# Performance work log

Hardware: AMD Instinct MI355X
Metric: run time of the kernel (lower is better)

Reference implementation:

```python
import jax, jax.numpy as jnp
import numpy as np

H = 512  # hidden size

def _lstm_layer(xseq, W_ih, W_hh, b_ih, b_hh):
    """xseq: [S,B,D]. Returns (h_seq [S,B,H], c_final [B,H]). PyTorch gate order i,f,g,o."""
    S, B, _ = xseq.shape
    # precompute input contribution for all timesteps: [S,B,4H]
    gx = jnp.einsum('sbd,gd->sbg', xseq, W_ih) + b_ih + b_hh
    h0 = jnp.zeros((B, H), xseq.dtype)
    c0 = jnp.zeros((B, H), xseq.dtype)

    def step(carry, gx_t):
        h, c = carry
        gates = gx_t + h @ W_hh.T  # [B,4H]
        i, f, g, o = jnp.split(gates, 4, axis=-1)
        c = jax.nn.sigmoid(f) * c + jax.nn.sigmoid(i) * jnp.tanh(g)
        h = jax.nn.sigmoid(o) * jnp.tanh(c)
        return (h, c), h

    (_, c_fin), h_seq = jax.lax.scan(step, (h0, c0), gx)
    return h_seq, c_fin


def setup_inputs() -> dict:
    key = jax.random.key(0)
    ks = jax.random.split(key, 12)
    V, D, L = 50257, 300, 10
    s = 0.08  # weight scale to keep gates in a sane range
    return {
        'x': jax.random.randint(ks[0], (64, 512), 0, V),
        'emb': jax.random.normal(ks[1], (V, D), jnp.float32),
        'W_ih0': s * jax.random.normal(ks[2], (4 * H, D), jnp.float32),
        'W_hh0': s * jax.random.normal(ks[3], (4 * H, H), jnp.float32),
        'b_ih0': s * jax.random.normal(ks[4], (4 * H,), jnp.float32),
        'b_hh0': s * jax.random.normal(ks[5], (4 * H,), jnp.float32),
        'W_ih1': s * jax.random.normal(ks[6], (4 * H, H), jnp.float32),
        'W_hh1': s * jax.random.normal(ks[7], (4 * H, H), jnp.float32),
        'b_ih1': s * jax.random.normal(ks[8], (4 * H,), jnp.float32),
        'b_hh1': s * jax.random.normal(ks[9], (4 * H,), jnp.float32),
        'W_out': s * jax.random.normal(ks[10], (L, H), jnp.float32),
        'b_out': s * jax.random.normal(ks[11], (L,), jnp.float32),
    }


def reference(x, emb, W_ih0, W_hh0, b_ih0, b_hh0, W_ih1, W_hh1, b_ih1, b_hh1, W_out, b_out):
    xe = emb[x]                      # [B,S,D] embedding gather
    xe = jnp.transpose(xe, (1, 0, 2))  # [S,B,D] time-major for scan
    h1, _ = _lstm_layer(xe, W_ih0, W_hh0, b_ih0, b_hh0)
    _, c2 = _lstm_layer(h1, W_ih1, W_hh1, b_ih1, b_hh1)  # c_n[-1]: [B,H]
    return c2 @ W_out.T + b_out      # [B,n_labels]
```

## Files before the change

kernel.cpp:

```cpp
#include <hip/hip_runtime.h>
#include <hip/hip_bf16.h>
#include <stdint.h>

#define BB 64
#define SS 512
#define HH 512
#define DD 300
#define DP 320

typedef __attribute__((ext_vector_type(8))) short short8;
typedef __attribute__((ext_vector_type(4))) float f32x4;

__device__ __forceinline__ unsigned short f2bf(float f) {
  unsigned u = __builtin_bit_cast(unsigned, f);
  u += 0x7fffu + ((u >> 16) & 1u);
  return (unsigned short)(u >> 16);
}
__device__ __forceinline__ float sigm(float x) { return 1.f / (1.f + __expf(-x)); }
__device__ __forceinline__ float tanh_f(float x) {
  float t = __expf(-2.f * fabsf(x));
  float r = (1.f - t) / (1.f + t);
  return x < 0.f ? -r : r;
}

__device__ __forceinline__ short8 load_frag_sc1(const unsigned short* p) {
  short8 r;
  asm volatile("global_load_dwordx4 %0, %1, off sc1" : "=v"(r) : "v"(p));
  return r;
}
__device__ __forceinline__ short8 load_frag(const unsigned short* p) {
  short8 r;
  asm volatile("global_load_dwordx4 %0, %1, off" : "=v"(r) : "v"(p));
  return r;
}

#define OFF_ARR   0u
#define OFF_EP    8192u
#define OFF_H1    16384u
#define OFF_H2    147456u
#define OFF_C2    278528u
#define OFF_XE    409600u
#define OFF_W0    21381120u
#define OFF_W1    24788992u
#define OFF_B0    28983296u
#define OFF_B1    28991488u
#define MEMSET_BYTES 278528u

__global__ void prep_weights(const float* __restrict__ Wih0, const float* __restrict__ Whh0,
                             const float* __restrict__ bih0, const float* __restrict__ bhh0,
                             const float* __restrict__ Wih1, const float* __restrict__ Whh1,
                             const float* __restrict__ bih1, const float* __restrict__ bhh1,
                             unsigned short* __restrict__ Wp0, unsigned short* __restrict__ Wp1,
                             float* __restrict__ b0p, float* __restrict__ b1p)
{
  int idx = blockIdx.x * 256 + threadIdx.x;
  int grow = idx >> 10;
  int k1 = idx & 1023;
  int l = grow & 31;
  int lb = grow >> 5;
  int gate = l >> 3;
  int orig = gate * 512 + lb * 8 + (l & 7);
  float v1 = (k1 < 512) ? Wih1[orig * 512 + k1] : Whh1[orig * 512 + (k1 - 512)];
  Wp1[idx] = f2bf(v1);
  if (k1 < 832) {
    float v0;
    if (k1 < 512)      v0 = Whh0[orig * 512 + k1];
    else if (k1 < 812) v0 = Wih0[orig * 300 + (k1 - 512)];
    else               v0 = 0.f;
    Wp0[grow * 832 + k1] = f2bf(v0);
  }
  if (k1 == 0) {
    b0p[grow] = bih0[orig] + bhh0[orig];
    b1p[grow] = bih1[orig] + bhh1[orig];
  }
}

__global__ void gather_xe(const int* __restrict__ x, const float* __restrict__ emb,
                          unsigned short* __restrict__ xe)
{
  int idx = blockIdx.x * 256 + threadIdx.x;
  int dk = idx % DP;
  int rem = idx / DP;
  int b = rem % BB;
  int t = rem / BB;
  int tok = x[b * SS + t];
  float v = (dk < DD) ? emb[(size_t)tok * DD + dk] : 0.f;
  size_t ua = (size_t)t * 20480 + (size_t)(dk >> 5) * 2048 + (size_t)(b >> 4) * 512
            + (size_t)((dk >> 3) & 3) * 128 + (size_t)(b & 15) * 8 + (dk & 7);
  xe[ua] = f2bf(v);
}

template<bool IS_L0>
__device__ __forceinline__ void scan_body(
    int blk,
    const unsigned short* __restrict__ xe,
    const unsigned short* __restrict__ Wp,
    const float* __restrict__ biasP,
    unsigned short* __restrict__ h1r,
    unsigned short* __restrict__ h2r,
    float* __restrict__ c2,
    unsigned int* cnt,
    float (&gl)[2][64][36], float (&bias_sm)[32])
{
  constexpr int K  = IS_L0 ? 832 : 1024;
  constexpr int NK = IS_L0 ? 13 : 16;

  const int tid  = threadIdx.x;
  const int lane = tid & 63;
  const int wave = tid >> 6;
  const int lrow = lane & 15;
  const int m    = wave & 3;
  const int q    = wave >> 2;
  const int lblk = IS_L0 ? blk : blk - 64;
  const int qkb  = q * NK;

  if (tid < 32) bias_sm[tid] = biasP[lblk * 32 + tid];

  short8 Bf0[NK], Bf1[NK];
  {
    const unsigned short* wr0 = Wp + (size_t)(lblk * 32 + lrow) * K + qkb * 32 + (lane >> 4) * 8;
    const unsigned short* wr1 = wr0 + (size_t)16 * K;
    #pragma unroll
    for (int j = 0; j < NK; ++j) {
      Bf0[j] = *(const short8*)(wr0 + j * 32);
      Bf1[j] = *(const short8*)(wr1 + j * 32);
    }
  }
  #pragma unroll
  for (int j = 0; j < NK; ++j)
    asm volatile("" : "+v"(Bf0[j]), "+v"(Bf1[j]));

  float creg = 0.f;
  const int pb = tid >> 3;
  const int ph = tid & 7;
  const size_t hst = (size_t)(lblk >> 2) * 2048 + (size_t)(pb >> 4) * 512
                   + (size_t)(lblk & 3) * 128 + (size_t)(pb & 15) * 8 + ph;

  for (int k = 0;; ++k) {
    const bool active = IS_L0 ? (k < 512) : (k >= 1);
    short8 a[NK];

    if (IS_L0 && active) {
      const unsigned short* xet = xe + (size_t)k * 20480;
      #pragma unroll
      for (int j = 0; j < NK; ++j) {
        const int kg = qkb + j;
        if (kg >= 16)
          a[j] = load_frag(xet + (size_t)(kg - 16) * 2048 + (size_t)m * 512 + lane * 8);
      }
    }

    if (k >= 1) {
      if (wave == 0) {
        const unsigned tgt = (unsigned)k * 8u;
        int guard = 0;
        for (;;) {
          unsigned v = (lane < 16)
              ? __hip_atomic_load(cnt + lane * 128, __ATOMIC_RELAXED, __HIP_MEMORY_SCOPE_AGENT)
              : tgt;
          if (__all(v >= tgt)) break;
          if (++guard > (1 << 18)) break;
        }
      }
      __syncthreads();
    }

    if (active) {
      const int t = IS_L0 ? k : k - 1;
      const unsigned short* hA = h1r + (size_t)((IS_L0 ? (t + 1) : t) & 1) * 32768;
      const unsigned short* hB = h2r + (size_t)((t + 1) & 1) * 32768;

      #pragma unroll
      for (int j = 0; j < NK; ++j) {
        const int kg = qkb + j;
        if (kg < 16) {
          a[j] = load_frag_sc1(hA + (size_t)kg * 2048 + (size_t)m * 512 + lane * 8);
        } else if (!IS_L0) {
          a[j] = load_frag_sc1(hB + (size_t)(kg - 16) * 2048 + (size_t)m * 512 + lane * 8);
        }
      }
      asm volatile("s_waitcnt vmcnt(0)" ::: "memory");
      __builtin_amdgcn_sched_barrier(0);

      f32x4 acc0 = {0.f, 0.f, 0.f, 0.f};
      f32x4 acc1 = {0.f, 0.f, 0.f, 0.f};
      #pragma unroll
      for (int j = 0; j < NK; ++j) {
        acc0 = __builtin_amdgcn_mfma_f32_16x16x32_bf16(a[j], Bf0[j], acc0, 0, 0, 0);
        acc1 = __builtin_amdgcn_mfma_f32_16x16x32_bf16(a[j], Bf1[j], acc1, 0, 0, 0);
      }
      #pragma unroll
      for (int r = 0; r < 4; ++r) {
        const int bb = m * 16 + (lane >> 4) * 4 + r;
        gl[q][bb][lrow]      = acc0[r];
        gl[q][bb][16 + lrow] = acc1[r];
      }
      __syncthreads();

      {
        float gi = gl[0][pb][ph]      + gl[1][pb][ph]      + bias_sm[ph];
        float gf = gl[0][pb][8 + ph]  + gl[1][pb][8 + ph]  + bias_sm[8 + ph];
        float gg = gl[0][pb][16 + ph] + gl[1][pb][16 + ph] + bias_sm[16 + ph];
        float go = gl[0][pb][24 + ph] + gl[1][pb][24 + ph] + bias_sm[24 + ph];
        float iv = sigm(gi), fv = sigm(gf), ov = sigm(go), gv = tanh_f(gg);
        creg = fv * creg + iv * gv;
        float hv = ov * tanh_f(creg);
        unsigned short hb = f2bf(hv);
        unsigned pair = (unsigned)hb | ((unsigned)(unsigned short)__shfl_down((int)hb, 1) << 16);
        unsigned short* hw = (IS_L0 ? h1r : h2r) + (size_t)(t & 1) * 32768 + hst;
        if ((ph & 1) == 0)
          __hip_atomic_store((unsigned*)hw, pair, __ATOMIC_RELAXED, __HIP_MEMORY_SCOPE_AGENT);
        if (!IS_L0 && k == 512) c2[pb * HH + lblk * 8 + ph] = creg;
      }
      asm volatile("s_waitcnt vmcnt(0)" ::: "memory");
    }

    if (k == 512) break;
    __syncthreads();
    if (tid == 0)
      __hip_atomic_fetch_add(cnt + (blk >> 3) * 128, 1u, __ATOMIC_RELAXED,
                             __HIP_MEMORY_SCOPE_AGENT);
  }
}

__attribute__((amdgpu_waves_per_eu(2, 2)))
__global__ void __launch_bounds__(512)
lstm_scan(const unsigned short* __restrict__ xe,
          const unsigned short* __restrict__ Wp0,
          const unsigned short* __restrict__ Wp1,
          const float* __restrict__ b0p, const float* __restrict__ b1p,
          unsigned short* __restrict__ h1r, unsigned short* __restrict__ h2r,
          float* __restrict__ c2, unsigned int* __restrict__ cnt)
{
  __shared__ float gl[2][64][36];
  __shared__ float bias_sm[32];
  const int blk = blockIdx.x;
  if (blk < 64) scan_body<true >(blk, xe, Wp0, b0p, h1r, h2r, c2, cnt, gl, bias_sm);
  else          scan_body<false>(blk, xe, Wp1, b1p, h1r, h2r, c2, cnt, gl, bias_sm);
}

__global__ void outproj(const float* __restrict__ c2, const float* __restrict__ Wout,
                        const float* __restrict__ bout, float* __restrict__ out)
{
  int t = threadIdx.x;
  if (t >= 640) return;
  int b = t / 10, l = t % 10;
  float s = bout[l];
  #pragma unroll 8
  for (int h = 0; h < 512; ++h) s += c2[b * 512 + h] * Wout[l * 512 + h];
  out[b * 10 + l] = s;
}

extern "C" void kernel_launch(void* const* d_in, const int* in_sizes, int n_in,
                              void* d_out, int out_size, void* d_ws, size_t ws_size,
                              hipStream_t stream) {
  (void)in_sizes; (void)n_in; (void)out_size; (void)ws_size;
  const int*   x    = (const int*)  d_in[0];
  const float* emb  = (const float*)d_in[1];
  const float* Wih0 = (const float*)d_in[2];
  const float* Whh0 = (const float*)d_in[3];
  const float* bih0 = (const float*)d_in[4];
  const float* bhh0 = (const float*)d_in[5];
  const float* Wih1 = (const float*)d_in[6];
  const float* Whh1 = (const float*)d_in[7];
  const float* bih1 = (const float*)d_in[8];
  const float* bhh1 = (const float*)d_in[9];
  const float* Wout = (const float*)d_in[10];
  const float* bout = (const float*)d_in[11];
  float* out = (float*)d_out;

  char* ws = (char*)d_ws;
  unsigned int*   cnt = (unsigned int*)  (ws + OFF_ARR);
  unsigned short* h1r = (unsigned short*)(ws + OFF_H1);
  unsigned short* h2r = (unsigned short*)(ws + OFF_H2);
  float*          c2  = (float*)         (ws + OFF_C2);
  unsigned short* xe  = (unsigned short*)(ws + OFF_XE);
  unsigned short* Wp0 = (unsigned short*)(ws + OFF_W0);
  unsigned short* Wp1 = (unsigned short*)(ws + OFF_W1);
  float*          b0p = (float*)         (ws + OFF_B0);
  float*          b1p = (float*)         (ws + OFF_B1);

  hipMemsetAsync(ws, 0, MEMSET_BYTES, stream);
  prep_weights<<<8192, 256, 0, stream>>>(Wih0, Whh0, bih0, bhh0, Wih1, Whh1, bih1, bhh1,
                                         Wp0, Wp1, b0p, b1p);
  gather_xe<<<40960, 256, 0, stream>>>(x, emb, xe);
  lstm_scan<<<128, 512, 0, stream>>>(xe, Wp0, Wp1, b0p, b1p, h1r, h2r, c2, cnt);
  outproj<<<1, 640, 0, stream>>>(c2, Wout, bout, out);
}
```

Before: 2.240 ms.

## Decouple LSTM layers with per-block sequence flags and 4-deep h1 ring

After: 1.916 ms. -14.4%, faster.

```diff
diff --git a/kernel.cpp b/kernel.cpp
--- a/kernel.cpp
+++ b/kernel.cpp
@@ -33,18 +33,23 @@
   asm volatile("global_load_dwordx4 %0, %1, off" : "=v"(r) : "v"(p));
   return r;
 }
-
-#define OFF_ARR   0u
-#define OFF_EP    8192u
-#define OFF_H1    16384u
-#define OFF_H2    147456u
-#define OFF_C2    278528u
-#define OFF_XE    409600u
-#define OFF_W0    21381120u
-#define OFF_W1    24788992u
-#define OFF_B0    28983296u
-#define OFF_B1    28991488u
-#define MEMSET_BYTES 278528u
+__device__ __forceinline__ unsigned ld_seq(const unsigned int* p) {
+  return __hip_atomic_load(p, __ATOMIC_RELAXED, __HIP_MEMORY_SCOPE_AGENT);
+}
+__device__ __forceinline__ void st_seq(unsigned int* p, unsigned v) {
+  __hip_atomic_store(p, v, __ATOMIC_RELAXED, __HIP_MEMORY_SCOPE_AGENT);
+}
+
+#define OFF_SEQ   0u
+#define OFF_H1    8192u
+#define OFF_H2    270336u
+#define OFF_C2    401408u
+#define OFF_XE    532480u
+#define OFF_W0    21504000u
+#define OFF_W1    24911872u
+#define OFF_B0    29106176u
+#define OFF_B1    29114368u
+#define MEMSET_BYTES 401408u
 
 __global__ void prep_weights(const float* __restrict__ Wih0, const float* __restrict__ Whh0,
                              const float* __restrict__ bih0, const float* __restrict__ bhh0,
@@ -90,28 +95,22 @@
   xe[ua] = f2bf(v);
 }
 
-template<bool IS_L0>
-__device__ __forceinline__ void scan_body(
-    int blk,
+__device__ __forceinline__ void scan_l0(
+    int lblk,
     const unsigned short* __restrict__ xe,
     const unsigned short* __restrict__ Wp,
     const float* __restrict__ biasP,
     unsigned short* __restrict__ h1r,
-    unsigned short* __restrict__ h2r,
-    float* __restrict__ c2,
-    unsigned int* cnt,
+    unsigned int* h1seq, unsigned int* l1seq,
     float (&gl)[2][64][36], float (&bias_sm)[32])
 {
-  constexpr int K  = IS_L0 ? 832 : 1024;
-  constexpr int NK = IS_L0 ? 13 : 16;
-
+  constexpr int K = 832, NK = 13;
   const int tid  = threadIdx.x;
   const int lane = tid & 63;
   const int wave = tid >> 6;
   const int lrow = lane & 15;
   const int m    = wave & 3;
   const int q    = wave >> 2;
-  const int lblk = IS_L0 ? blk : blk - 64;
   const int qkb  = q * NK;
 
   if (tid < 32) bias_sm[tid] = biasP[lblk * 32 + tid];
@@ -127,8 +126,7 @@
     }
   }
   #pragma unroll
-  for (int j = 0; j < NK; ++j)
-    asm volatile("" : "+v"(Bf0[j]), "+v"(Bf1[j]));
+  for (int j = 0; j < NK; ++j) asm volatile("" : "+v"(Bf0[j]), "+v"(Bf1[j]));
 
   float creg = 0.f;
   const int pb = tid >> 3;
@@ -136,12 +134,10 @@
   const size_t hst = (size_t)(lblk >> 2) * 2048 + (size_t)(pb >> 4) * 512
                    + (size_t)(lblk & 3) * 128 + (size_t)(pb & 15) * 8 + ph;
 
-  for (int k = 0;; ++k) {
-    const bool active = IS_L0 ? (k < 512) : (k >= 1);
+  for (int t = 0; t < 512; ++t) {
     short8 a[NK];
-
-    if (IS_L0 && active) {
-      const unsigned short* xet = xe + (size_t)k * 20480;
+    {
+      const unsigned short* xet = xe + (size_t)t * 20480;
       #pragma unroll
       for (int j = 0; j < NK; ++j) {
         const int kg = qkb + j;
@@ -149,39 +145,126 @@
           a[j] = load_frag(xet + (size_t)(kg - 16) * 2048 + (size_t)m * 512 + lane * 8);
       }
     }
-
-    if (k >= 1) {
+    if (t >= 1) {
       if (wave == 0) {
-        const unsigned tgt = (unsigned)k * 8u;
         int guard = 0;
         for (;;) {
-          unsigned v = (lane < 16)
-              ? __hip_atomic_load(cnt + lane * 128, __ATOMIC_RELAXED, __HIP_MEMORY_SCOPE_AGENT)
-              : tgt;
-          if (__all(v >= tgt)) break;
-          if (++guard > (1 << 18)) break;
+          unsigned v1 = ld_seq(h1seq + lane * 16);
+          unsigned v2 = ld_seq(l1seq + lane * 16);
+          bool ok = (v1 >= (unsigned)t) && ((int)v2 >= t - 3);
+          if (__all(ok)) break;
+          if (++guard > (1 << 20)) break;
+          __builtin_amdgcn_s_sleep(1);
         }
       }
       __syncthreads();
     }
-
-    if (active) {
-      const int t = IS_L0 ? k : k - 1;
-      const unsigned short* hA = h1r + (size_t)((IS_L0 ? (t + 1) : t) & 1) * 32768;
-      const unsigned short* hB = h2r + (size_t)((t + 1) & 1) * 32768;
-
+    {
+      const unsigned short* hA = h1r + (size_t)((t + 3) & 3) * 32768;
       #pragma unroll
       for (int j = 0; j < NK; ++j) {
         const int kg = qkb + j;
-        if (kg < 16) {
+        if (kg < 16)
           a[j] = load_frag_sc1(hA + (size_t)kg * 2048 + (size_t)m * 512 + lane * 8);
-        } else if (!IS_L0) {
-          a[j] = load_frag_sc1(hB + (size_t)(kg - 16) * 2048 + (size_t)m * 512 + lane * 8);
-        }
-      }
+      }
+    }
+    asm volatile("s_waitcnt vmcnt(0)" ::: "memory");
+    __builtin_amdgcn_sched_barrier(0);
+
+    f32x4 acc0 = {0.f, 0.f, 0.f, 0.f};
+    f32x4 acc1 = {0.f, 0.f, 0.f, 0.f};
+    #pragma unroll
+    for (int j = 0; j < NK; ++j) {
+      acc0 = __builtin_amdgcn_mfma_f32_16x16x32_bf16(a[j], Bf0[j], acc0, 0, 0, 0);
+      acc1 = __builtin_amdgcn_mfma_f32_16x16x32_bf16(a[j], Bf1[j], acc1, 0, 0, 0);
+    }
+    #pragma unroll
+    for (int r = 0; r < 4; ++r) {
+      const int bb = m * 16 + (lane >> 4) * 4 + r;
+      gl[q][bb][lrow]      = acc0[r];
+      gl[q][bb][16 + lrow] = acc1[r];
+    }
+    __syncthreads();
+    {
+      float gi = gl[0][pb][ph]      + gl[1][pb][ph]      + bias_sm[ph];
+      float gf = gl[0][pb][8 + ph]  + gl[1][pb][8 + ph]  + bias_sm[8 + ph];
+      float gg = gl[0][pb][16 + ph] + gl[1][pb][16 + ph] + bias_sm[16 + ph];
+      float go = gl[0][pb][24 + ph] + gl[1][pb][24 + ph] + bias_sm[24 + ph];
+      float iv = sigm(gi), fv = sigm(gf), ov = sigm(go), gv = tanh_f(gg);
+      creg = fv * creg + iv * gv;
+      float hv = ov * tanh_f(creg);
+      unsigned short hb = f2bf(hv);
+      unsigned pair = (unsigned)hb | ((unsigned)(unsigned short)__shfl_down((int)hb, 1) << 16);
+      unsigned short* hw = h1r + (size_t)(t & 3) * 32768 + hst;
+      if ((ph & 1) == 0)
+        __hip_atomic_store((unsigned*)hw, pair, __ATOMIC_RELAXED, __HIP_MEMORY_SCOPE_AGENT);
+    }
+    asm volatile("s_waitcnt vmcnt(0)" ::: "memory");
+    __syncthreads();
+    if (tid == 0) st_seq(h1seq + lblk * 16, (unsigned)(t + 1));
+  }
+}
+
+__device__ __forceinline__ void scan_l1(
+    int lblk,
+    const unsigned short* __restrict__ Wp,
+    const float* __restrict__ biasP,
+    const unsigned short* __restrict__ h1r,
+    unsigned short* __restrict__ h2r,
+    float* __restrict__ c2,
+    unsigned int* h1seq, unsigned int* l1seq,
+    float (&gl)[2][64][36], float (&bias_sm)[32])
+{
+  constexpr int K = 1024, NK = 16;
+  const int tid  = threadIdx.x;
+  const int lane = tid & 63;
+  const int wave = tid >> 6;
+  const int lrow = lane & 15;
+  const int m    = wave & 3;
+  const int q    = wave >> 2;
+  const int qkb  = q * NK;
+
+  if (tid < 32) bias_sm[tid] = biasP[lblk * 32 + tid];
+
+  short8 Bf0[NK], Bf1[NK];
+  {
+    const unsigned short* wr0 = Wp + (size_t)(lblk * 32 + lrow) * K + qkb * 32 + (lane >> 4) * 8;
+    const unsigned short* wr1 = wr0 + (size_t)16 * K;
+    #pragma unroll
+    for (int j = 0; j < NK; ++j) {
+      Bf0[j] = *(const short8*)(wr0 + j * 32);
+      Bf1[j] = *(const short8*)(wr1 + j * 32);
+    }
+  }
+  #pragma unroll
+  for (int j = 0; j < NK; ++j) asm volatile("" : "+v"(Bf0[j]), "+v"(Bf1[j]));
+
+  float creg = 0.f;
+  const int pb = tid >> 3;
+  const int ph = tid & 7;
+  const size_t hst = (size_t)(lblk >> 2) * 2048 + (size_t)(pb >> 4) * 512
+                   + (size_t)(lblk & 3) * 128 + (size_t)(pb & 15) * 8 + ph;
+
+  for (int t = 0; t < 512; ++t) {
+    if (wave == 0) {
+      int guard = 0;
+      for (;;) {
+        unsigned v = ld_seq(h1seq + lane * 16);
+        if (__all(v >= (unsigned)(t + 1))) break;
+        if (++guard > (1 << 20)) break;
+        __builtin_amdgcn_s_sleep(1);
+      }
+    }
+    __syncthreads();
+
+    if (q == 0) {
+      const unsigned short* hA = h1r + (size_t)(t & 3) * 32768;
+      short8 a[NK];
+      #pragma unroll
+      for (int j = 0; j < NK; ++j)
+        a[j] = load_frag_sc1(hA + (size_t)j * 2048 + (size_t)m * 512 + lane * 8);
       asm volatile("s_waitcnt vmcnt(0)" ::: "memory");
       __builtin_amdgcn_sched_barrier(0);
-
       f32x4 acc0 = {0.f, 0.f, 0.f, 0.f};
       f32x4 acc1 = {0.f, 0.f, 0.f, 0.f};
       #pragma unroll
@@ -192,34 +275,62 @@
       #pragma unroll
       for (int r = 0; r < 4; ++r) {
         const int bb = m * 16 + (lane >> 4) * 4 + r;
-        gl[q][bb][lrow]      = acc0[r];
-        gl[q][bb][16 + lrow] = acc1[r];
-      }
-      __syncthreads();
-
-      {
-        float gi = gl[0][pb][ph]      + gl[1][pb][ph]      + bias_sm[ph];
-        float gf = gl[0][pb][8 + ph]  + gl[1][pb][8 + ph]  + bias_sm[8 + ph];
-        float gg = gl[0][pb][16 + ph] + gl[1][pb][16 + ph] + bias_sm[16 + ph];
-        float go = gl[0][pb][24 + ph] + gl[1][pb][24 + ph] + bias_sm[24 + ph];
-        float iv = sigm(gi), fv = sigm(gf), ov = sigm(go), gv = tanh_f(gg);
-        creg = fv * creg + iv * gv;
-        float hv = ov * tanh_f(creg);
-        unsigned short hb = f2bf(hv);
-        unsigned pair = (unsigned)hb | ((unsigned)(unsigned short)__shfl_down((int)hb, 1) << 16);
-        unsigned short* hw = (IS_L0 ? h1r : h2r) + (size_t)(t & 1) * 32768 + hst;
-        if ((ph & 1) == 0)
-          __hip_atomic_store((unsigned*)hw, pair, __ATOMIC_RELAXED, __HIP_MEMORY_SCOPE_AGENT);
-        if (!IS_L0 && k == 512) c2[pb * HH + lblk * 8 + ph] = creg;
-      }
+        gl[0][bb][lrow]      = acc0[r];
+        gl[0][bb][16 + lrow] = acc1[r];
+      }
+    } else if (wave == 4) {
+      int guard = 0;
+      for (;;) {
+        unsigned v = ld_seq(l1seq + lane * 16);
+        if (__all(v >= (unsigned)t)) break;
+        if (++guard > (1 << 20)) break;
+        __builtin_amdgcn_s_sleep(1);
+      }
+    }
+    __syncthreads();
+
+    if (q == 1) {
+      const unsigned short* hB = h2r + (size_t)((t + 1) & 1) * 32768;
+      short8 a[NK];
+      #pragma unroll
+      for (int j = 0; j < NK; ++j)
+        a[j] = load_frag_sc1(hB + (size_t)j * 2048 + (size_t)m * 512 + lane * 8);
       asm volatile("s_waitcnt vmcnt(0)" ::: "memory");
-    }
-
-    if (k == 512) break;
-    __syncthreads();
-    if (tid == 0)
-      __hip_atomic_fetch_add(cnt + (blk >> 3) * 128, 1u, __ATOMIC_RELAXED,
-                             __HIP_MEMORY_SCOPE_AGENT);
+      __builtin_amdgcn_sched_barrier(0);
+      f32x4 acc0 = {0.f, 0.f, 0.f, 0.f};
+      f32x4 acc1 = {0.f, 0.f, 0.f, 0.f};
+      #pragma unroll
+      for (int j = 0; j < NK; ++j) {
+        acc0 = __builtin_amdgcn_mfma_f32_16x16x32_bf16(a[j], Bf0[j], acc0, 0, 0, 0);
+        acc1 = __builtin_amdgcn_mfma_f32_16x16x32_bf16(a[j], Bf1[j], acc1, 0, 0, 0);
+      }
+      #pragma unroll
+      for (int r = 0; r < 4; ++r) {
+        const int bb = m * 16 + (lane >> 4) * 4 + r;
+        gl[1][bb][lrow]      = acc0[r];
+        gl[1][bb][16 + lrow] = acc1[r];
+      }
+    }
+    __syncthreads();
+
+    {
+      float gi = gl[0][pb][ph]      + gl[1][pb][ph]      + bias_sm[ph];
+      float gf = gl[0][pb][8 + ph]  + gl[1][pb][8 + ph]  + bias_sm[8 + ph];
+      float gg = gl[0][pb][16 + ph] + gl[1][pb][16 + ph] + bias_sm[16 + ph];
+      float go = gl[0][pb][24 + ph] + gl[1][pb][24 + ph] + bias_sm[24 + ph];
+      float iv = sigm(gi), fv = sigm(gf), ov = sigm(go), gv = tanh_f(gg);
+      creg = fv * creg + iv * gv;
+      float hv = ov * tanh_f(creg);
+      unsigned short hb = f2bf(hv);
+      unsigned pair = (unsigned)hb | ((unsigned)(unsigned short)__shfl_down((int)hb, 1) << 16);
+      unsigned short* hw = h2r + (size_t)(t & 1) * 32768 + hst;
+      if ((ph & 1) == 0)
+        __hip_atomic_store((unsigned*)hw, pair, __ATOMIC_RELAXED, __HIP_MEMORY_SCOPE_AGENT);
+      if (t == 511) c2[pb * HH + lblk * 8 + ph] = creg;
+    }
+    asm volatile("s_waitcnt vmcnt(0)" ::: "memory");
+    __syncthreads();
+    if (tid == 0) st_seq(l1seq + lblk * 16, (unsigned)(t + 1));
   }
 }
 
@@ -230,13 +341,15 @@
           const unsigned short* __restrict__ Wp1,
           const float* __restrict__ b0p, const float* __restrict__ b1p,
           unsigned short* __restrict__ h1r, unsigned short* __restrict__ h2r,
-          float* __restrict__ c2, unsigned int* __restrict__ cnt)
+          float* __restrict__ c2, unsigned int* __restrict__ seqbase)
 {
   __shared__ float gl[2][64][36];
   __shared__ float bias_sm[32];
+  unsigned int* h1seq = seqbase;
+  unsigned int* l1seq = seqbase + 1024;
   const int blk = blockIdx.x;
-  if (blk < 64) scan_body<true >(blk, xe, Wp0, b0p, h1r, h2r, c2, cnt, gl, bias_sm);
-  else          scan_body<false>(blk, xe, Wp1, b1p, h1r, h2r, c2, cnt, gl, bias_sm);
+  if (blk < 64) scan_l0(blk,      xe, Wp0, b0p, h1r, h1seq, l1seq, gl, bias_sm);
+  else          scan_l1(blk - 64, Wp1, b1p, h1r, h2r, c2, h1seq, l1seq, gl, bias_sm);
 }
 
 __global__ void outproj(const float* __restrict__ c2, const float* __restrict__ Wout,
@@ -270,20 +383,20 @@
   float* out = (float*)d_out;
 
   char* ws = (char*)d_ws;
-  unsigned int*   cnt = (unsigned int*)  (ws + OFF_ARR);
-  unsigned short* h1r = (unsigned short*)(ws + OFF_H1);
-  unsigned short* h2r = (unsigned short*)(ws + OFF_H2);
-  float*          c2  = (float*)         (ws + OFF_C2);
-  unsigned short* xe  = (unsigned short*)(ws + OFF_XE);
-  unsigned short* Wp0 = (unsigned short*)(ws + OFF_W0);
-  unsigned short* Wp1 = (unsigned short*)(ws + OFF_W1);
-  float*          b0p = (float*)         (ws + OFF_B0);
-  float*          b1p = (float*)         (ws + OFF_B1);
+  unsigned int*   seqb = (unsigned int*)  (ws + OFF_SEQ);
+  unsigned short* h1r  = (unsigned short*)(ws + OFF_H1);
+  unsigned short* h2r  = (unsigned short*)(ws + OFF_H2);
+  float*          c2   = (float*)         (ws + OFF_C2);
+  unsigned short* xe   = (unsigned short*)(ws + OFF_XE);
+  unsigned short* Wp0  = (unsigned short*)(ws + OFF_W0);
+  unsigned short* Wp1  = (unsigned short*)(ws + OFF_W1);
+  float*          b0p  = (float*)         (ws + OFF_B0);
+  float*          b1p  = (float*)         (ws + OFF_B1);
 
   hipMemsetAsync(ws, 0, MEMSET_BYTES, stream);
   prep_weights<<<8192, 256, 0, stream>>>(Wih0, Whh0, bih0, bhh0, Wih1, Whh1, bih1, bhh1,
                                          Wp0, Wp1, b0p, b1p);
   gather_xe<<<40960, 256, 0, stream>>>(x, emb, xe);
-  lstm_scan<<<128, 512, 0, stream>>>(xe, Wp0, Wp1, b0p, b1p, h1r, h2r, c2, cnt);
+  lstm_scan<<<128, 512, 0, stream>>>(xe, Wp0, Wp1, b0p, b1p, h1r, h2r, c2, seqb);
   outproj<<<1, 640, 0, stream>>>(c2, Wout, bout, out);
 }
```

## Replace global counter barrier with per-element tagged h polling and ring buffers

Applied to the files above, without the earlier changes.

Result: slower. 5.752 ms (+156.8%).

```diff
diff --git a/kernel.cpp b/kernel.cpp
--- a/kernel.cpp
+++ b/kernel.cpp
@@ -10,6 +10,7 @@
 
 typedef __attribute__((ext_vector_type(8))) short short8;
 typedef __attribute__((ext_vector_type(4))) float f32x4;
+typedef __attribute__((ext_vector_type(4))) unsigned int u32x4;
 
 __device__ __forceinline__ unsigned short f2bf(float f) {
   unsigned u = __builtin_bit_cast(unsigned, f);
@@ -23,28 +24,33 @@
   return x < 0.f ? -r : r;
 }
 
-__device__ __forceinline__ short8 load_frag_sc1(const unsigned short* p) {
-  short8 r;
-  asm volatile("global_load_dwordx4 %0, %1, off sc1" : "=v"(r) : "v"(p));
-  return r;
-}
 __device__ __forceinline__ short8 load_frag(const unsigned short* p) {
   short8 r;
   asm volatile("global_load_dwordx4 %0, %1, off" : "=v"(r) : "v"(p));
   return r;
 }
-
-#define OFF_ARR   0u
-#define OFF_EP    8192u
-#define OFF_H1    16384u
-#define OFF_H2    147456u
-#define OFF_C2    278528u
-#define OFF_XE    409600u
-#define OFF_W0    21381120u
-#define OFF_W1    24788992u
-#define OFF_B0    28983296u
-#define OFF_B1    28991488u
-#define MEMSET_BYTES 278528u
+__device__ __forceinline__ u32x4 load_u4_sc1(const unsigned int* p) {
+  u32x4 r;
+  asm volatile("global_load_dwordx4 %0, %1, off sc1" : "=v"(r) : "v"(p));
+  return r;
+}
+__device__ __forceinline__ unsigned ld_seq(const unsigned int* p) {
+  return __hip_atomic_load(p, __ATOMIC_RELAXED, __HIP_MEMORY_SCOPE_AGENT);
+}
+__device__ __forceinline__ void st_u32(unsigned int* p, unsigned v) {
+  __hip_atomic_store(p, v, __ATOMIC_RELAXED, __HIP_MEMORY_SCOPE_AGENT);
+}
+
+#define OFF_SEQ   0u
+#define OFF_H1    8192u
+#define OFF_H2    532480u
+#define OFF_C2    794624u
+#define OFF_XE    925696u
+#define OFF_W0    21897216u
+#define OFF_W1    25305088u
+#define OFF_B0    29499392u
+#define OFF_B1    29507584u
+#define MEMSET_BYTES 794624u
 
 __global__ void prep_weights(const float* __restrict__ Wih0, const float* __restrict__ Whh0,
                              const float* __restrict__ bih0, const float* __restrict__ bhh0,
@@ -90,136 +96,197 @@
   xe[ua] = f2bf(v);
 }
 
-template<bool IS_L0>
-__device__ __forceinline__ void scan_body(
-    int blk,
+template<int G>
+__device__ __forceinline__ void poll_frags(const unsigned int* __restrict__ slot,
+                                           int kg0, int m, int lane, unsigned tagw,
+                                           short8* aout)
+{
+  const unsigned int* base = slot + (size_t)kg0 * 2048 + (size_t)m * 512 + (size_t)lane * 8;
+  u32x4 lo[G], hi[G];
+  int guard = 0;
+  for (;;) {
+    #pragma unroll
+    for (int j = 0; j < G; ++j) {
+      lo[j] = load_u4_sc1(base + (size_t)j * 2048);
+      hi[j] = load_u4_sc1(base + (size_t)j * 2048 + 4);
+    }
+    asm volatile("s_waitcnt vmcnt(0)" ::: "memory");
+    __builtin_amdgcn_sched_barrier(0);
+    unsigned orv = 0;
+    #pragma unroll
+    for (int j = 0; j < G; ++j) {
+      orv |= (lo[j].x ^ tagw) | (lo[j].y ^ tagw) | (lo[j].z ^ tagw) | (lo[j].w ^ tagw)
+           | (hi[j].x ^ tagw) | (hi[j].y ^ tagw) | (hi[j].z ^ tagw) | (hi[j].w ^ tagw);
+    }
+    if (__all((orv >> 16) == 0u)) break;
+    if (++guard > (1 << 15)) break;
+    __builtin_amdgcn_s_sleep(1);
+  }
+  #pragma unroll
+  for (int j = 0; j < G; ++j) {
+    union { short8 s; unsigned u[4]; } o;
+    o.u[0] = (lo[j].x & 0xFFFFu) | (lo[j].y << 16);
+    o.u[1] = (lo[j].z & 0xFFFFu) | (lo[j].w << 16);
+    o.u[2] = (hi[j].x & 0xFFFFu) | (hi[j].y << 16);
+    o.u[3] = (hi[j].z & 0xFFFFu) | (hi[j].w << 16);
+    aout[j] = o.s;
+  }
+}
+
+__device__ __forceinline__ void scan_l0(
+    int lblk,
     const unsigned short* __restrict__ xe,
     const unsigned short* __restrict__ Wp,
     const float* __restrict__ biasP,
-    unsigned short* __restrict__ h1r,
-    unsigned short* __restrict__ h2r,
-    float* __restrict__ c2,
-    unsigned int* cnt,
-    float (&gl)[2][64][36], float (&bias_sm)[32])
-{
-  constexpr int K  = IS_L0 ? 832 : 1024;
-  constexpr int NK = IS_L0 ? 13 : 16;
-
+    unsigned int* __restrict__ h1p,
+    const unsigned int* __restrict__ l1seq,
+    float (&gl)[2][2][64][36], float (&bias_sm)[32])
+{
+  constexpr int K = 832;
   const int tid  = threadIdx.x;
   const int lane = tid & 63;
   const int wave = tid >> 6;
   const int lrow = lane & 15;
   const int m    = wave & 3;
   const int q    = wave >> 2;
-  const int lblk = IS_L0 ? blk : blk - 64;
-  const int qkb  = q * NK;
+  const int qkb  = q * 13;
 
   if (tid < 32) bias_sm[tid] = biasP[lblk * 32 + tid];
 
-  short8 Bf0[NK], Bf1[NK];
-  {
-    const unsigned short* wr0 = Wp + (size_t)(lblk * 32 + lrow) * K + qkb * 32 + (lane >> 4) * 8;
-    const unsigned short* wr1 = wr0 + (size_t)16 * K;
-    #pragma unroll
-    for (int j = 0; j < NK; ++j) {
-      Bf0[j] = *(const short8*)(wr0 + j * 32);
-      Bf1[j] = *(const short8*)(wr1 + j * 32);
-    }
-  }
-  #pragma unroll
-  for (int j = 0; j < NK; ++j)
-    asm volatile("" : "+v"(Bf0[j]), "+v"(Bf1[j]));
+  const unsigned short* wr0 = Wp + (size_t)(lblk * 32 + lrow) * K + qkb * 32 + (lane >> 4) * 8;
+  const unsigned short* wr1 = wr0 + (size_t)16 * K;
 
   float creg = 0.f;
   const int pb = tid >> 3;
   const int ph = tid & 7;
-  const size_t hst = (size_t)(lblk >> 2) * 2048 + (size_t)(pb >> 4) * 512
-                   + (size_t)(lblk & 3) * 128 + (size_t)(pb & 15) * 8 + ph;
-
-  for (int k = 0;; ++k) {
-    const bool active = IS_L0 ? (k < 512) : (k >= 1);
-    short8 a[NK];
-
-    if (IS_L0 && active) {
-      const unsigned short* xet = xe + (size_t)k * 20480;
+  const size_t hstu = (size_t)(lblk >> 2) * 2048 + (size_t)(pb >> 4) * 512
+                    + (size_t)(lblk & 3) * 128 + (size_t)(pb & 15) * 8 + ph;
+
+  for (int t = 0; t < 512; ++t) {
+    short8 a[13];
+    if (q == 1) {
+      const unsigned short* xet = xe + (size_t)t * 20480;
       #pragma unroll
-      for (int j = 0; j < NK; ++j) {
-        const int kg = qkb + j;
-        if (kg >= 16)
-          a[j] = load_frag(xet + (size_t)(kg - 16) * 2048 + (size_t)m * 512 + lane * 8);
+      for (int j = 3; j < 13; ++j)
+        a[j] = load_frag(xet + (size_t)(qkb + j - 16) * 2048 + (size_t)m * 512 + lane * 8);
+    }
+    {
+      const unsigned int* slotR = h1p + (size_t)((t + 3) & 3) * 32768;
+      const unsigned tagw = (unsigned)t << 16;
+      if (q == 0) poll_frags<13>(slotR, 0,  m, lane, tagw, a);
+      else        poll_frags<3 >(slotR, 13, m, lane, tagw, a);
+    }
+    f32x4 acc0 = {0.f, 0.f, 0.f, 0.f};
+    f32x4 acc1 = {0.f, 0.f, 0.f, 0.f};
+    #pragma unroll
+    for (int j = 0; j < 13; ++j) {
+      short8 b0 = *(const short8*)(wr0 + j * 32);
+      short8 b1 = *(const short8*)(wr1 + j * 32);
+      acc0 = __builtin_amdgcn_mfma_f32_16x16x32_bf16(a[j], b0, acc0, 0, 0, 0);
+      acc1 = __builtin_amdgcn_mfma_f32_16x16x32_bf16(a[j], b1, acc1, 0, 0, 0);
+    }
+    #pragma unroll
+    for (int r = 0; r < 4; ++r) {
+      const int bb = m * 16 + (lane >> 4) * 4 + r;
+      gl[t & 1][q][bb][lrow]      = acc0[r];
+      gl[t & 1][q][bb][16 + lrow] = acc1[r];
+    }
+    if (wave == 0) {
+      int guard = 0;
+      for (;;) {
+        unsigned v = ld_seq(l1seq + lane * 16);
+        if (__all((int)v >= t - 3)) break;
+        if (++guard > (1 << 15)) break;
+        __builtin_amdgcn_s_sleep(4);
       }
     }
-
-    if (k >= 1) {
-      if (wave == 0) {
-        const unsigned tgt = (unsigned)k * 8u;
-        int guard = 0;
-        for (;;) {
-          unsigned v = (lane < 16)
-              ? __hip_atomic_load(cnt + lane * 128, __ATOMIC_RELAXED, __HIP_MEMORY_SCOPE_AGENT)
-              : tgt;
-          if (__all(v >= tgt)) break;
-          if (++guard > (1 << 18)) break;
-        }
-      }
-      __syncthreads();
-    }
-
-    if (active) {
-      const int t = IS_L0 ? k : k - 1;
-      const unsigned short* hA = h1r + (size_t)((IS_L0 ? (t + 1) : t) & 1) * 32768;
-      const unsigned short* hB = h2r + (size_t)((t + 1) & 1) * 32768;
-
-      #pragma unroll
-      for (int j = 0; j < NK; ++j) {
-        const int kg = qkb + j;
-        if (kg < 16) {
-          a[j] = load_frag_sc1(hA + (size_t)kg * 2048 + (size_t)m * 512 + lane * 8);
-        } else if (!IS_L0) {
-          a[j] = load_frag_sc1(hB + (size_t)(kg - 16) * 2048 + (size_t)m * 512 + lane * 8);
-        }
-      }
-      asm volatile("s_waitcnt vmcnt(0)" ::: "memory");
-      __builtin_amdgcn_sched_barrier(0);
-
-      f32x4 acc0 = {0.f, 0.f, 0.f, 0.f};
-      f32x4 acc1 = {0.f, 0.f, 0.f, 0.f};
-      #pragma unroll
-      for (int j = 0; j < NK; ++j) {
-        acc0 = __builtin_amdgcn_mfma_f32_16x16x32_bf16(a[j], Bf0[j], acc0, 0, 0, 0);
-        acc1 = __builtin_amdgcn_mfma_f32_16x16x32_bf16(a[j], Bf1[j], acc1, 0, 0, 0);
-      }
-      #pragma unroll
-      for (int r = 0; r < 4; ++r) {
-        const int bb = m * 16 + (lane >> 4) * 4 + r;
-        gl[q][bb][lrow]      = acc0[r];
-        gl[q][bb][16 + lrow] = acc1[r];
-      }
-      __syncthreads();
-
-      {
-        float gi = gl[0][pb][ph]      + gl[1][pb][ph]      + bias_sm[ph];
-        float gf = gl[0][pb][8 + ph]  + gl[1][pb][8 + ph]  + bias_sm[8 + ph];
-        float gg = gl[0][pb][16 + ph] + gl[1][pb][16 + ph] + bias_sm[16 + ph];
-        float go = gl[0][pb][24 + ph] + gl[1][pb][24 + ph] + bias_sm[24 + ph];
-        float iv = sigm(gi), fv = sigm(gf), ov = sigm(go), gv = tanh_f(gg);
-        creg = fv * creg + iv * gv;
-        float hv = ov * tanh_f(creg);
-        unsigned short hb = f2bf(hv);
-        unsigned pair = (unsigned)hb | ((unsigned)(unsigned short)__shfl_down((int)hb, 1) << 16);
-        unsigned short* hw = (IS_L0 ? h1r : h2r) + (size_t)(t & 1) * 32768 + hst;
-        if ((ph & 1) == 0)
-          __hip_atomic_store((unsigned*)hw, pair, __ATOMIC_RELAXED, __HIP_MEMORY_SCOPE_AGENT);
-        if (!IS_L0 && k == 512) c2[pb * HH + lblk * 8 + ph] = creg;
-      }
-      asm volatile("s_waitcnt vmcnt(0)" ::: "memory");
-    }
-
-    if (k == 512) break;
     __syncthreads();
-    if (tid == 0)
-      __hip_atomic_fetch_add(cnt + (blk >> 3) * 128, 1u, __ATOMIC_RELAXED,
-                             __HIP_MEMORY_SCOPE_AGENT);
+    {
+      const float* g0 = gl[t & 1][0][pb];
+      const float* g1 = gl[t & 1][1][pb];
+      float gi = g0[ph]      + g1[ph]      + bias_sm[ph];
+      float gf = g0[8 + ph]  + g1[8 + ph]  + bias_sm[8 + ph];
+      float gg = g0[16 + ph] + g1[16 + ph] + bias_sm[16 + ph];
+      float go = g0[24 + ph] + g1[24 + ph] + bias_sm[24 + ph];
+      float iv = sigm(gi), fv = sigm(gf), ov = sigm(go), gv = tanh_f(gg);
+      creg = fv * creg + iv * gv;
+      float hv = ov * tanh_f(creg);
+      unsigned val = ((unsigned)(t + 1) << 16) | f2bf(hv);
+      st_u32(h1p + (size_t)(t & 3) * 32768 + hstu, val);
+    }
+  }
+}
+
+__device__ __forceinline__ void scan_l1(
+    int lblk,
+    const unsigned short* __restrict__ Wp,
+    const float* __restrict__ biasP,
+    const unsigned int* __restrict__ h1p,
+    unsigned int* __restrict__ h2p,
+    float* __restrict__ c2,
+    unsigned int* __restrict__ l1seq,
+    float (&gl)[2][2][64][36], float (&bias_sm)[32])
+{
+  constexpr int K = 1024;
+  const int tid  = threadIdx.x;
+  const int lane = tid & 63;
+  const int wave = tid >> 6;
+  const int lrow = lane & 15;
+  const int m    = wave & 3;
+  const int q    = wave >> 2;
+  const int qkb  = q * 16;
+
+  if (tid < 32) bias_sm[tid] = biasP[lblk * 32 + tid];
+
+  const unsigned short* wr0 = Wp + (size_t)(lblk * 32 + lrow) * K + qkb * 32 + (lane >> 4) * 8;
+  const unsigned short* wr1 = wr0 + (size_t)16 * K;
+
+  float creg = 0.f;
+  const int pb = tid >> 3;
+  const int ph = tid & 7;
+  const size_t hstu = (size_t)(lblk >> 2) * 2048 + (size_t)(pb >> 4) * 512
+                    + (size_t)(lblk & 3) * 128 + (size_t)(pb & 15) * 8 + ph;
+
+  for (int t = 0; t < 512; ++t) {
+    short8 a[16];
+    if (q == 0) {
+      const unsigned int* slotR = h1p + (size_t)(t & 3) * 32768;
+      poll_frags<16>(slotR, 0, m, lane, (unsigned)(t + 1) << 16, a);
+    } else {
+      const unsigned int* slotR = h2p + (size_t)((t + 1) & 1) * 32768;
+      poll_frags<16>(slotR, 0, m, lane, (unsigned)t << 16, a);
+    }
+    f32x4 acc0 = {0.f, 0.f, 0.f, 0.f};
+    f32x4 acc1 = {0.f, 0.f, 0.f, 0.f};
+    #pragma unroll
+    for (int j = 0; j < 16; ++j) {
+      short8 b0 = *(const short8*)(wr0 + j * 32);
+      short8 b1 = *(const short8*)(wr1 + j * 32);
+      acc0 = __builtin_amdgcn_mfma_f32_16x16x32_bf16(a[j], b0, acc0, 0, 0, 0);
+      acc1 = __builtin_amdgcn_mfma_f32_16x16x32_bf16(a[j], b1, acc1, 0, 0, 0);
+    }
+    #pragma unroll
+    for (int r = 0; r < 4; ++r) {
+      const int bb = m * 16 + (lane >> 4) * 4 + r;
+      gl[t & 1][q][bb][lrow]      = acc0[r];
+      gl[t & 1][q][bb][16 + lrow] = acc1[r];
+    }
+    __syncthreads();
+    if (tid == 0) st_u32(l1seq + lblk * 16, (unsigned)(t + 1));
+    {
+      const float* g0 = gl[t & 1][0][pb];
+      const float* g1 = gl[t & 1][1][pb];
+      float gi = g0[ph]      + g1[ph]      + bias_sm[ph];
+      float gf = g0[8 + ph]  + g1[8 + ph]  + bias_sm[8 + ph];
+      float gg = g0[16 + ph] + g1[16 + ph] + bias_sm[16 + ph];
+      float go = g0[24 + ph] + g1[24 + ph] + bias_sm[24 + ph];
+      float iv = sigm(gi), fv = sigm(gf), ov = sigm(go), gv = tanh_f(gg);
+      creg = fv * creg + iv * gv;
+      float hv = ov * tanh_f(creg);
+      unsigned val = ((unsigned)(t + 1) << 16) | f2bf(hv);
+      st_u32(h2p + (size_t)(t & 1) * 32768 + hstu, val);
+      if (t == 511) c2[pb * HH + lblk * 8 + ph] = creg;
+    }
   }
 }
 
@@ -229,14 +296,14 @@
           const unsigned short* __restrict__ Wp0,
           const unsigned short* __restrict__ Wp1,
           const float* __restrict__ b0p, const float* __restrict__ b1p,
-          unsigned short* __restrict__ h1r, unsigned short* __restrict__ h2r,
-          float* __restrict__ c2, unsigned int* __restrict__ cnt)
-{
-  __shared__ float gl[2][64][36];
+          unsigned int* __restrict__ h1p, unsigned int* __restrict__ h2p,
+          float* __restrict__ c2, unsigned int* __restrict__ l1seq)
+{
+  __shared__ float gl[2][2][64][36];
   __shared__ float bias_sm[32];
   const int blk = blockIdx.x;
-  if (blk < 64) scan_body<true >(blk, xe, Wp0, b0p, h1r, h2r, c2, cnt, gl, bias_sm);
-  else          scan_body<false>(blk, xe, Wp1, b1p, h1r, h2r, c2, cnt, gl, bias_sm);
+  if (blk < 64) scan_l0(blk,      xe, Wp0, b0p, h1p, l1seq, gl, bias_sm);
+  else          scan_l1(blk - 64, Wp1, b1p, h1p, h2p, c2, l1seq, gl, bias_sm);
 }
 
 __global__ void outproj(const float* __restrict__ c2, const float* __restrict__ Wout,
@@ -270,9 +337,9 @@
   float* out = (float*)d_out;
 
   char* ws = (char*)d_ws;
-  unsigned int*   cnt = (unsigned int*)  (ws + OFF_ARR);
-  unsigned short* h1r = (unsigned short*)(ws + OFF_H1);
-  unsigned short* h2r = (unsigned short*)(ws + OFF_H2);
+  unsigned int*   l1s = (unsigned int*)  (ws + OFF_SEQ);
+  unsigned int*   h1p = (unsigned int*)  (ws + OFF_H1);
+  unsigned int*   h2p = (unsigned int*)  (ws + OFF_H2);
   float*          c2  = (float*)         (ws + OFF_C2);
   unsigned short* xe  = (unsigned short*)(ws + OFF_XE);
   unsigned short* Wp0 = (unsigned short*)(ws + OFF_W0);
@@ -284,6 +351,6 @@
   prep_weights<<<8192, 256, 0, stream>>>(Wih0, Whh0, bih0, bhh0, Wih1, Whh1, bih1, bhh1,
                                          Wp0, Wp1, b0p, b1p);
   gather_xe<<<40960, 256, 0, stream>>>(x, emb, xe);
-  lstm_scan<<<128, 512, 0, stream>>>(xe, Wp0, Wp1, b0p, b1p, h1r, h2r, c2, cnt);
+  lstm_scan<<<128, 512, 0, stream>>>(xe, Wp0, Wp1, b0p, b1p, h1p, h2p, c2, l1s);
   outproj<<<1, 640, 0, stream>>>(c2, Wout, bout, out);
 }
```
